# Performance work log

Measured on AMD Instinct MI355X. Metric: run time of the kernel, lower is better.

Reference implementation:

```python
import jax, jax.numpy as jnp
import numpy as np

# Grid constants from voxel_size=(0.2,0.2,4), point_cloud_range=(0,-40,-3,70.4,40,1)
VX, VY, VZ = 0.2, 0.2, 4.0
PCR = (0.0, -40.0, -3.0, 70.4, 40.0, 1.0)
NX, NY, NZ = 352, 400, 1   # round((hi-lo)/v) per axis
BATCH = 2
N_POINTS = 400000
CANVAS = BATCH * NZ * NY * NX  # dense canvas of all voxels (segment ids)
EPS = 1e-3  # BN1d eps from norm_cfg


def _vidx(coors):
    # linear voxel index: b*Z*Y*X + z*Y*X + y*X + x  (coors = [b,z,y,x])
    c = coors.astype(jnp.int32)
    return ((c[:, 0] * NZ + c[:, 1]) * NY + c[:, 2]) * NX + c[:, 3]


def _seg_mean(x, idx):
    # scatter-mean over voxels (DynamicScatter, average_points=True)
    s = jax.ops.segment_sum(x, idx, num_segments=CANVAS)
    c = jax.ops.segment_sum(jnp.ones((x.shape[0], 1), x.dtype), idx, num_segments=CANVAS)
    return s / jnp.maximum(c, 1.0)


def _seg_max(x, idx):
    # scatter-max over voxels (DynamicScatter, average_points=False); empty voxels -> 0
    m = jax.ops.segment_max(x, idx, num_segments=CANVAS)
    c = jax.ops.segment_sum(jnp.ones((x.shape[0],), x.dtype), idx, num_segments=CANVAS)
    return jnp.where((c > 0)[:, None], m, jnp.zeros_like(m))


def _bn_relu(x, g, b):
    # BN1d in training mode (batch stats, biased var), affine, then ReLU
    mu = x.mean(axis=0)
    var = x.var(axis=0)
    return jax.nn.relu((x - mu) * jax.lax.rsqrt(var + EPS) * g + b)


def setup_inputs() -> dict:
    key = jax.random.key(0)
    ks = jax.random.split(key, 6)
    features = jax.random.normal(ks[0], (N_POINTS, 4), jnp.float32)
    # coors [b, z, y, x]; batch column sorted so coors[-1,0]+1 == batch_size
    half = N_POINTS // 2
    b = jnp.concatenate([jnp.zeros(half, jnp.int32), jnp.ones(N_POINTS - half, jnp.int32)])
    z = jnp.zeros(N_POINTS, jnp.int32)  # NZ == 1
    y = jax.random.randint(ks[1], (N_POINTS,), 0, NY, jnp.int32)
    x = jax.random.randint(ks[2], (N_POINTS,), 0, NX, jnp.int32)
    coors = jnp.stack([b, z, y, x], axis=1)
    # VFE params: layer0 Linear(10->64, no bias), layer1 Linear(128->128, no bias)
    W0 = jax.random.normal(ks[3], (10, 64), jnp.float32) * 0.1
    g0 = jnp.ones((64,), jnp.float32)
    b0 = jnp.zeros((64,), jnp.float32)
    W1 = jax.random.normal(ks[4], (128, 128), jnp.float32) * 0.1
    g1 = jnp.ones((128,), jnp.float32)
    b1 = jnp.zeros((128,), jnp.float32)
    return {"features": features, "coors": coors, "W0": W0, "g0": g0, "b0": b0,
            "W1": W1, "g1": g1, "b1": b1}


def reference(features, coors, W0, g0, b0, W1, g1, b1):
    idx = _vidx(coors)
    # cluster center: scatter-mean of point features, gather back to points
    vmean = _seg_mean(features, idx)
    pts_mean = vmean[idx]
    f_cluster = features[:, :3] - pts_mean[:, :3]
    # voxel center offset
    cf = coors.astype(features.dtype)
    f_center = jnp.stack([
        features[:, 0] - (cf[:, 3] * VX + (VX / 2 + PCR[0])),
        features[:, 1] - (cf[:, 2] * VY + (VY / 2 + PCR[1])),
        features[:, 2] - (cf[:, 1] * VZ + (VZ / 2 + PCR[2])),
    ], axis=1)
    feat = jnp.concatenate([features, f_cluster, f_center], axis=1)  # (N, 10)
    # VFE layer 0 + voxel max pool + gather-broadcast + concat
    pf0 = _bn_relu(feat @ W0, g0, b0)           # (N, 64)
    v0 = _seg_max(pf0, idx)                     # (CANVAS, 64)
    feat1 = jnp.concatenate([pf0, v0[idx]], axis=1)  # (N, 128)
    # VFE layer 1 + final voxel max pool
    pf1 = _bn_relu(feat1 @ W1, g1, b1)          # (N, 128)
    voxel_feats = _seg_max(pf1, idx)            # (CANVAS, 128), dense canvas
    return voxel_feats
```

## Files before the change

kernel.cpp:

```cpp
#include <hip/hip_runtime.h>

#define NPTS 400000
#define NXv 352
#define NYv 400
#define CANVAS 281600
#define G2B 512
#define SCANB 275

typedef unsigned int uint;
typedef unsigned short ushort;
typedef __attribute__((ext_vector_type(8))) short short8;
typedef __attribute__((ext_vector_type(4))) float floatx4;

__device__ inline uint packbf(float a, float b) {
    uint ua = __float_as_uint(a);
    ua = (ua + 0x7fffu + ((ua >> 16) & 1u)) >> 16;
    uint ub = __float_as_uint(b);
    ub = (ub + 0x7fffu + ((ub >> 16) & 1u)) & 0xffff0000u;
    return ua | ub;
}
__device__ inline ushort bf16bits(float a) {
    uint u = __float_as_uint(a);
    return (ushort)((u + 0x7fffu + ((u >> 16) & 1u)) >> 16);
}
__device__ inline float lo16(uint u) { return __uint_as_float(u << 16); }
__device__ inline float hi16(uint u) { return __uint_as_float(u & 0xffff0000u); }
__device__ inline float bfval(ushort u) { return __uint_as_float(((uint)u) << 16); }

__global__ void k_bucket(const int4* __restrict__ coors, const float* __restrict__ W1,
                         int* __restrict__ idxbuf, int* __restrict__ pidx,
                         uint* __restrict__ ucnt, ushort* __restrict__ w1t) {
    int b = blockIdx.x;
    if (b < 1563) {
        int i = b * 256 + threadIdx.x;
        if (i >= NPTS) return;
        int4 c = coors[i];
        int idx = ((c.x + c.y) * NYv + c.z) * NXv + c.w;
        idxbuf[i] = idx;
        pidx[i] = (int)atomicAdd(&ucnt[idx], 1u);
    } else {
        int i = (b - 1563) * 256 + threadIdx.x;
        int n = i & 127, k = i >> 7;
        w1t[n * 128 + k] = bf16bits(W1[k * 128 + n]);
    }
}

__global__ __launch_bounds__(1024) void k_scanA(const uint* __restrict__ ucnt,
                                                uint* __restrict__ voff,
                                                uint* __restrict__ bsum) {
    __shared__ uint sh[1024];
    int t = threadIdx.x;
    int v = blockIdx.x * 1024 + t;
    uint val = ucnt[v];
    sh[t] = val;
    for (int off = 1; off < 1024; off <<= 1) {
        __syncthreads();
        uint x = (t >= off) ? sh[t - off] : 0u;
        __syncthreads();
        sh[t] += x;
    }
    uint incl = sh[t];
    voff[v] = incl - val;
    if (t == 1023) bsum[blockIdx.x] = incl;
}

__global__ __launch_bounds__(1024) void k_scanC(const uint* __restrict__ bsum,
                                                uint* __restrict__ voff) {
    __shared__ uint sh[1024];
    __shared__ uint bs[1024];
    int t = threadIdx.x;
    uint val = (t < SCANB) ? bsum[t] : 0u;
    sh[t] = val; bs[t] = val;
    for (int off = 1; off < 1024; off <<= 1) {
        __syncthreads();
        uint x = (t >= off) ? sh[t - off] : 0u;
        __syncthreads();
        sh[t] += x;
    }
    __syncthreads();
    uint off_ = sh[blockIdx.x] - bs[blockIdx.x];
    int v = blockIdx.x * 1024 + t;
    voff[v] += off_;
    if (blockIdx.x == SCANB - 1 && t == 1023) voff[CANVAS] = NPTS;
}

__global__ void k_perm(const int* __restrict__ idxbuf, const int* __restrict__ pidx,
                       const uint* __restrict__ voff, const float4* __restrict__ feat,
                       int* __restrict__ vidx, float4* __restrict__ featS) {
    int i = blockIdx.x * 256 + threadIdx.x;
    if (i >= NPTS) return;
    int idx = idxbuf[i];
    uint j = voff[idx] + (uint)pidx[i];
    vidx[j] = idx;
    featS[j] = feat[i];
}

__global__ void k_vmean(const float4* __restrict__ featS, const uint* __restrict__ voff,
                        float4* __restrict__ vmean) {
    int v = blockIdx.x * 256 + threadIdx.x;
    if (v >= CANVAS) return;
    uint s_ = voff[v], e_ = voff[v + 1];
    float4 s = make_float4(0.f, 0.f, 0.f, 0.f);
    for (uint j = s_; j < e_; ++j) {
        float4 f = featS[j];
        s.x += f.x; s.y += f.y; s.z += f.z; s.w += f.w;
    }
    float inv = 1.0f / (float)max((int)(e_ - s_), 1);
    vmean[v] = make_float4(s.x * inv, s.y * inv, s.z * inv, s.w * inv);
}

__global__ __launch_bounds__(256) void k_gemm1(
        const float4* __restrict__ featS, const int* __restrict__ vidx,
        const float4* __restrict__ vmean, const float* __restrict__ W0,
        uint* __restrict__ x0u, float* __restrict__ stats) {
    __shared__ float w0s[640];
    __shared__ __align__(8) ushort tile[256 * 68];
    __shared__ float ps[128], qs[128];
    for (int t = threadIdx.x; t < 640; t += 256) w0s[t] = W0[t];
    __syncthreads();
    int j = blockIdx.x * 256 + threadIdx.x;
    bool valid = j < NPTS;
    ushort* trow = &tile[threadIdx.x * 68];
    if (valid) {
        float4 f = featS[j];
        int idx = vidx[j];
        float4 vm = vmean[idx];
        int xq = idx % NXv;
        int yq = (idx / NXv) % NYv;
        float ft[10];
        ft[0] = f.x; ft[1] = f.y; ft[2] = f.z; ft[3] = f.w;
        ft[4] = f.x - vm.x;
        ft[5] = f.y - vm.y;
        ft[6] = f.z - vm.z;
        ft[7] = f.x - ((float)xq * 0.2f + 0.1f);
        ft[8] = f.y - ((float)yq * 0.2f - 39.9f);
        ft[9] = f.z + 1.0f;
        uint* o = x0u + (size_t)j * 32;
        #pragma unroll
        for (int g = 0; g < 8; ++g) {
            float a[8];
            #pragma unroll
            for (int q = 0; q < 8; ++q) a[q] = 0.f;
            #pragma unroll
            for (int k = 0; k < 10; ++k) {
                float fk = ft[k];
                #pragma unroll
                for (int q = 0; q < 8; ++q) a[q] = fmaf(fk, w0s[k * 64 + g * 8 + q], a[q]);
            }
            uint4 w;
            w.x = packbf(a[0], a[1]); w.y = packbf(a[2], a[3]);
            w.z = packbf(a[4], a[5]); w.w = packbf(a[6], a[7]);
            *(uint4*)(o + g * 4) = w;
            ((uint2*)trow)[g * 2 + 0] = make_uint2(w.x, w.y);
            ((uint2*)trow)[g * 2 + 1] = make_uint2(w.z, w.w);
        }
    } else {
        #pragma unroll
        for (int g = 0; g < 16; ++g) ((uint2*)trow)[g] = make_uint2(0u, 0u);
    }
    __syncthreads();
    if (threadIdx.x < 128) {
        int c = threadIdx.x & 63, half = threadIdx.x >> 6;
        float s = 0.f, q = 0.f;
        for (int r = half * 128; r < half * 128 + 128; ++r) {
            float xv = bfval(tile[r * 68 + c]);
            s += xv;
            q = fmaf(xv, xv, q);
        }
        ps[half * 64 + c] = s;
        qs[half * 64 + c] = q;
    }
    __syncthreads();
    if (threadIdx.x < 64) {
        int c = threadIdx.x;
        atomicAdd(&stats[c], ps[c] + ps[64 + c]);
        atomicAdd(&stats[64 + c], qs[c] + qs[64 + c]);
    }
}

__global__ void k_vmax0(const uint* __restrict__ x0u, const uint* __restrict__ voff,
                        const float* __restrict__ stats, const float* __restrict__ g0,
                        const float* __restrict__ b0, uint* __restrict__ v0u) {
    __shared__ float s[128];
    if (threadIdx.x < 64) {
        int c = threadIdx.x;
        float mu = stats[c] * (1.0f / NPTS);
        float var = stats[64 + c] * (1.0f / NPTS) - mu * mu;
        float sc = (1.0f / sqrtf(var + 1e-3f)) * g0[c];
        s[c] = sc;
        s[64 + c] = fmaf(-mu, sc, b0[c]);
    }
    __syncthreads();
    int t = blockIdx.x * 256 + threadIdx.x;
    int v = t >> 4;
    if (v >= CANVAS) return;
    uint s_ = voff[v], e_ = voff[v + 1];
    if (s_ == e_) return;
    int c = (t & 15) << 2;
    float4 m = make_float4(0.f, 0.f, 0.f, 0.f);
    for (uint j = s_; j < e_; ++j) {
        uint2 u = *(const uint2*)(x0u + (size_t)j * 32 + (c >> 1));
        m.x = fmaxf(m.x, fmaf(lo16(u.x), s[c + 0], s[64 + c + 0]));
        m.y = fmaxf(m.y, fmaf(hi16(u.x), s[c + 1], s[64 + c + 1]));
        m.z = fmaxf(m.z, fmaf(lo16(u.y), s[c + 2], s[64 + c + 2]));
        m.w = fmaxf(m.w, fmaf(hi16(u.y), s[c + 3], s[64 + c + 3]));
    }
    uint2 o; o.x = packbf(m.x, m.y); o.y = packbf(m.z, m.w);
    *(uint2*)(v0u + (size_t)v * 32 + (c >> 1)) = o;
}

__global__ __launch_bounds__(256) void k_gemm2p(
        const uint* __restrict__ x0u, const uint* __restrict__ v0u,
        const int* __restrict__ vidx, const uint* __restrict__ voff,
        const float* __restrict__ stats, const float* __restrict__ g0,
        const float* __restrict__ b0, const ushort* __restrict__ w1t,
        ushort* __restrict__ vmaxc, float* __restrict__ sums) {
    __shared__ __align__(16) ushort Bs[128 * 136];
    __shared__ __align__(16) ushort As[64 * 136];
    __shared__ __align__(16) ushort Cs[64 * 136];
    __shared__ float s[128];
    __shared__ int svid[2][64];

    for (int i = threadIdx.x; i < 2048; i += 256) {
        int r = i >> 4, ch = i & 15;
        *(uint4*)&Bs[r * 136 + ch * 8] = *(const uint4*)&w1t[r * 128 + ch * 8];
    }
    if (threadIdx.x < 64) {
        int c = threadIdx.x;
        float mu = stats[c] * (1.0f / NPTS);
        float var = stats[64 + c] * (1.0f / NPTS) - mu * mu;
        float sc = (1.0f / sqrtf(var + 1e-3f)) * g0[c];
        s[c] = sc;
        s[64 + c] = fmaf(-mu, sc, b0[c]);
    }

    int p0 = (int)((long long)blockIdx.x * NPTS / G2B);
    int p1 = (int)((long long)(blockIdx.x + 1) * NPTS / G2B);
    int ps, pe;
    { int v = vidx[p0]; ps = (voff[v] == (uint)p0) ? p0 : (int)voff[v + 1]; }
    if (p1 >= NPTS) pe = NPTS;
    else { int v = vidx[p1]; pe = (voff[v] == (uint)p1) ? p1 : (int)voff[v + 1]; }

    int lane = threadIdx.x & 63, wid = threadIdx.x >> 6;
    int m = lane & 15, q = lane >> 4;
    float run = -3.0e38f, csum = 0.f, csq = 0.f;
    int vcur = -1;
    __syncthreads();

    int sp = 0;
    for (int r0 = ps; r0 < pe; r0 += 64, sp ^= 1) {
        int nrows = min(64, pe - r0);
        for (int i = threadIdx.x; i < 512; i += 256) {
            int r = i >> 3, ch = i & 7, cb = ch * 8;
            uint4 o4 = make_uint4(0u, 0u, 0u, 0u);
            if (r < nrows) {
                uint4 u = *(const uint4*)(x0u + (size_t)(r0 + r) * 32 + ch * 4);
                uint w[4] = {u.x, u.y, u.z, u.w}, o[4];
                #pragma unroll
                for (int q2 = 0; q2 < 4; ++q2) {
                    float a = fmaxf(fmaf(lo16(w[q2]), s[cb + 2 * q2], s[64 + cb + 2 * q2]), 0.f);
                    float b = fmaxf(fmaf(hi16(w[q2]), s[cb + 2 * q2 + 1], s[64 + cb + 2 * q2 + 1]), 0.f);
                    o[q2] = packbf(a, b);
                }
                o4 = make_uint4(o[0], o[1], o[2], o[3]);
            }
            *(uint4*)&As[r * 136 + ch * 8] = o4;
        }
        for (int i = threadIdx.x; i < 512; i += 256) {
            int r = i >> 3, ch = i & 7;
            uint4 u = make_uint4(0u, 0u, 0u, 0u);
            if (r < nrows) u = *(const uint4*)(v0u + (size_t)vidx[r0 + r] * 32 + ch * 4);
            *(uint4*)&As[r * 136 + 64 + ch * 8] = u;
        }
        if (threadIdx.x < 64)
            svid[sp][threadIdx.x] = (threadIdx.x < nrows) ? vidx[r0 + threadIdx.x] : -1;
        __syncthreads();

        const ushort* ar = &As[(wid * 16 + m) * 136 + q * 8];
        short8 a0 = *(const short8*)&ar[0];
        short8 a1 = *(const short8*)&ar[32];
        short8 a2 = *(const short8*)&ar[64];
        short8 a3 = *(const short8*)&ar[96];
        #pragma unroll
        for (int ct = 0; ct < 8; ++ct) {
            const ushort* br = &Bs[(ct * 16 + m) * 136 + q * 8];
            short8 b0v = *(const short8*)&br[0];
            short8 b1v = *(const short8*)&br[32];
            short8 b2v = *(const short8*)&br[64];
            short8 b3v = *(const short8*)&br[96];
            floatx4 acc = {0.f, 0.f, 0.f, 0.f};
            acc = __builtin_amdgcn_mfma_f32_16x16x32_bf16(a0, b0v, acc, 0, 0, 0);
            acc = __builtin_amdgcn_mfma_f32_16x16x32_bf16(a1, b1v, acc, 0, 0, 0);
            acc = __builtin_amdgcn_mfma_f32_16x16x32_bf16(a2, b2v, acc, 0, 0, 0);
            acc = __builtin_amdgcn_mfma_f32_16x16x32_bf16(a3, b3v, acc, 0, 0, 0);
            #pragma unroll
            for (int rg = 0; rg < 4; ++rg)
                Cs[(wid * 16 + q * 4 + rg) * 136 + ct * 16 + m] = bf16bits(acc[rg]);
        }
        __syncthreads();

        if (threadIdx.x < 128) {
            int c = threadIdx.x;
            #pragma unroll 4
            for (int r = 0; r < 64; ++r) {
                int v = svid[sp][r];
                float x = bfval(Cs[r * 136 + c]);
                if (v != vcur) {
                    if (vcur >= 0) vmaxc[(size_t)vcur * 128 + c] = bf16bits(run);
                    vcur = v;
                    run = -3.0e38f;
                }
                if (v >= 0) {
                    run = fmaxf(run, x);
                    csum += x;
                    csq = fmaf(x, x, csq);
                }
            }
        }
    }
    if (threadIdx.x < 128) {
        if (vcur >= 0) vmaxc[(size_t)vcur * 128 + threadIdx.x] = bf16bits(run);
        atomicAdd(&sums[threadIdx.x], csum);
        atomicAdd(&sums[128 + threadIdx.x], csq);
    }
}

__global__ __launch_bounds__(256) void k_bnout(const ushort* __restrict__ vmaxc,
        const uint* __restrict__ voff, const float* __restrict__ stats,
        const float* __restrict__ g1, const float* __restrict__ b1,
        float4* __restrict__ out) {
    __shared__ float s[256];
    if (threadIdx.x < 128) {
        int c = threadIdx.x;
        float mu = stats[128 + c] * (1.0f / NPTS);
        float var = stats[256 + c] * (1.0f / NPTS) - mu * mu;
        float sc = (1.0f / sqrtf(var + 1e-3f)) * g1[c];
        s[c] = sc;
        s[128 + c] = fmaf(-mu, sc, b1[c]);
    }
    __syncthreads();
    int t = blockIdx.x * 256 + threadIdx.x;
    int v = t >> 5;
    if (v >= CANVAS) return;
    int c = (t & 31) << 2;
    float4 m = make_float4(0.f, 0.f, 0.f, 0.f);
    if (voff[v + 1] != voff[v]) {
        uint2 u = *(const uint2*)(vmaxc + (size_t)v * 128 + c);
        m.x = fmaxf(fmaf(lo16(u.x), s[c + 0], s[128 + c + 0]), 0.f);
        m.y = fmaxf(fmaf(hi16(u.x), s[c + 1], s[128 + c + 1]), 0.f);
        m.z = fmaxf(fmaf(lo16(u.y), s[c + 2], s[128 + c + 2]), 0.f);
        m.w = fmaxf(fmaf(hi16(u.y), s[c + 3], s[128 + c + 3]), 0.f);
    }
    out[(size_t)v * 32 + (c >> 2)] = m;
}

extern "C" void kernel_launch(void* const* d_in, const int* in_sizes, int n_in,
                              void* d_out, int out_size, void* d_ws, size_t ws_size,
                              hipStream_t stream) {
    const float4* feat  = (const float4*)d_in[0];
    const int4*   coors = (const int4*)d_in[1];
    const float*  W0    = (const float*)d_in[2];
    const float*  g0    = (const float*)d_in[3];
    const float*  b0    = (const float*)d_in[4];
    const float*  W1    = (const float*)d_in[5];
    const float*  g1    = (const float*)d_in[6];
    const float*  b1    = (const float*)d_in[7];

    char* ws = (char*)d_ws;
    int*    idxbuf = (int*)(ws + 0);
    int*    pidx   = (int*)(ws + 1600000);
    uint*   ucnt   = (uint*)(ws + 3200000);
    float*  stats  = (float*)(ws + 4326400);
    uint*   voff   = (uint*)(ws + 4329472);
    uint*   bsum   = (uint*)(ws + 5455888);
    int*    vidx   = (int*)(ws + 5459984);
    float*  featS  = (float*)(ws + 7059984);
    float*  vmean  = (float*)(ws + 13459984);
    ushort* w1t    = (ushort*)(ws + 17965584);
    uint*   x0u    = (uint*)(ws + 17998352);
    uint*   v0u    = (uint*)(ws + 69198352);
    ushort* vmaxc  = (ushort*)(ws + 105243152);

    hipMemsetAsync(ws + 3200000, 0, 1129472, stream);

    const int BLK = 256;
    int gpts = (NPTS + BLK - 1) / BLK;
    int gvox = (CANVAS + BLK - 1) / BLK;

    k_bucket<<<gpts + 64, BLK, 0, stream>>>(coors, W1, idxbuf, pidx, ucnt, w1t);
    k_scanA<<<SCANB, 1024, 0, stream>>>(ucnt, voff, bsum);
    k_scanC<<<SCANB, 1024, 0, stream>>>(bsum, voff);
    k_perm<<<gpts, BLK, 0, stream>>>(idxbuf, pidx, voff, feat, vidx, (float4*)featS);
    k_vmean<<<gvox, BLK, 0, stream>>>((const float4*)featS, voff, (float4*)vmean);
    k_gemm1<<<gpts, BLK, 0, stream>>>((const float4*)featS, vidx, (const float4*)vmean,
                                      W0, x0u, stats);
    k_vmax0<<<CANVAS * 16 / BLK, BLK, 0, stream>>>(x0u, voff, stats, g0, b0, v0u);
    k_gemm2p<<<G2B, BLK, 0, stream>>>(x0u, v0u, vidx, voff, stats, g0, b0, w1t,
                                      vmaxc, stats + 128);
    k_bnout<<<CANVAS * 32 / BLK, BLK, 0, stream>>>(vmaxc, voff, stats, g1, b1,
                                                   (float4*)d_out);
}
```

Before: 478.9 us.

## Hold W1 in registers and overlap next-tile staging with voxel max reduction

The second VFE GEMM kernel now loads each wave's W1 fragments directly into registers once, instead of copying W1 into LDS and re-reading it for every tile. Work within the block is specialized: threads 0-127 stage the next 64-row tile (BN0+ReLU of pf0 plus the gathered voxel max) while threads 128-255 run the per-voxel max and the BN-statistics reduction on the current tile. The reduction loop is also made branch-light by resetting the running max inline. The cost is about 128 extra VGPRs per thread, which may lower occupancy, and an extra barrier per tile.

Result: faster. 449.4 us (-6.2%).

```diff
diff --git a/kernel.cpp b/kernel.cpp
--- a/kernel.cpp
+++ b/kernel.cpp
@@ -215,16 +215,14 @@
         const float* __restrict__ stats, const float* __restrict__ g0,
         const float* __restrict__ b0, const ushort* __restrict__ w1t,
         ushort* __restrict__ vmaxc, float* __restrict__ sums) {
-    __shared__ __align__(16) ushort Bs[128 * 136];
     __shared__ __align__(16) ushort As[64 * 136];
     __shared__ __align__(16) ushort Cs[64 * 136];
     __shared__ float s[128];
     __shared__ int svid[2][64];
 
-    for (int i = threadIdx.x; i < 2048; i += 256) {
-        int r = i >> 4, ch = i & 15;
-        *(uint4*)&Bs[r * 136 + ch * 8] = *(const uint4*)&w1t[r * 128 + ch * 8];
-    }
+    int lane = threadIdx.x & 63, wid = threadIdx.x >> 6;
+    int m = lane & 15, q = lane >> 4;
+
     if (threadIdx.x < 64) {
         int c = threadIdx.x;
         float mu = stats[c] * (1.0f / NPTS);
@@ -234,6 +232,15 @@
         s[64 + c] = fmaf(-mu, sc, b0[c]);
     }
 
+    short8 breg[8][4];
+    #pragma unroll
+    for (int ct = 0; ct < 8; ++ct) {
+        const ushort* br = &w1t[(ct * 16 + m) * 128 + q * 8];
+        #pragma unroll
+        for (int ks = 0; ks < 4; ++ks)
+            breg[ct][ks] = *(const short8*)&br[ks * 32];
+    }
+
     int p0 = (int)((long long)blockIdx.x * NPTS / G2B);
     int p1 = (int)((long long)(blockIdx.x + 1) * NPTS / G2B);
     int ps, pe;
@@ -241,20 +248,16 @@
     if (p1 >= NPTS) pe = NPTS;
     else { int v = vidx[p1]; pe = (voff[v] == (uint)p1) ? p1 : (int)voff[v + 1]; }
 
-    int lane = threadIdx.x & 63, wid = threadIdx.x >> 6;
-    int m = lane & 15, q = lane >> 4;
     float run = -3.0e38f, csum = 0.f, csq = 0.f;
     int vcur = -1;
-    __syncthreads();
-
-    int sp = 0;
-    for (int r0 = ps; r0 < pe; r0 += 64, sp ^= 1) {
-        int nrows = min(64, pe - r0);
-        for (int i = threadIdx.x; i < 512; i += 256) {
+
+    auto stage = [&](int r0s, int p) {
+        int nrows = min(64, pe - r0s);
+        for (int i = threadIdx.x; i < 512; i += 128) {
             int r = i >> 3, ch = i & 7, cb = ch * 8;
             uint4 o4 = make_uint4(0u, 0u, 0u, 0u);
             if (r < nrows) {
-                uint4 u = *(const uint4*)(x0u + (size_t)(r0 + r) * 32 + ch * 4);
+                uint4 u = *(const uint4*)(x0u + (size_t)(r0s + r) * 32 + ch * 4);
                 uint w[4] = {u.x, u.y, u.z, u.w}, o[4];
                 #pragma unroll
                 for (int q2 = 0; q2 < 4; ++q2) {
@@ -266,16 +269,22 @@
             }
             *(uint4*)&As[r * 136 + ch * 8] = o4;
         }
-        for (int i = threadIdx.x; i < 512; i += 256) {
+        for (int i = threadIdx.x; i < 512; i += 128) {
             int r = i >> 3, ch = i & 7;
             uint4 u = make_uint4(0u, 0u, 0u, 0u);
-            if (r < nrows) u = *(const uint4*)(v0u + (size_t)vidx[r0 + r] * 32 + ch * 4);
+            if (r < nrows) u = *(const uint4*)(v0u + (size_t)vidx[r0s + r] * 32 + ch * 4);
             *(uint4*)&As[r * 136 + 64 + ch * 8] = u;
         }
         if (threadIdx.x < 64)
-            svid[sp][threadIdx.x] = (threadIdx.x < nrows) ? vidx[r0 + threadIdx.x] : -1;
-        __syncthreads();
-
+            svid[p][threadIdx.x] = (threadIdx.x < nrows) ? vidx[r0s + threadIdx.x] : -1;
+    };
+
+    __syncthreads();
+    if (threadIdx.x < 128 && ps < pe) stage(ps, 0);
+    __syncthreads();
+
+    int sp = 0;
+    for (int r0 = ps; r0 < pe; r0 += 64, sp ^= 1) {
         const ushort* ar = &As[(wid * 16 + m) * 136 + q * 8];
         short8 a0 = *(const short8*)&ar[0];
         short8 a1 = *(const short8*)&ar[32];
@@ -283,16 +292,11 @@
         short8 a3 = *(const short8*)&ar[96];
         #pragma unroll
         for (int ct = 0; ct < 8; ++ct) {
-            const ushort* br = &Bs[(ct * 16 + m) * 136 + q * 8];
-            short8 b0v = *(const short8*)&br[0];
-            short8 b1v = *(const short8*)&br[32];
-            short8 b2v = *(const short8*)&br[64];
-            short8 b3v = *(const short8*)&br[96];
             floatx4 acc = {0.f, 0.f, 0.f, 0.f};
-            acc = __builtin_amdgcn_mfma_f32_16x16x32_bf16(a0, b0v, acc, 0, 0, 0);
-            acc = __builtin_amdgcn_mfma_f32_16x16x32_bf16(a1, b1v, acc, 0, 0, 0);
-            acc = __builtin_amdgcn_mfma_f32_16x16x32_bf16(a2, b2v, acc, 0, 0, 0);
-            acc = __builtin_amdgcn_mfma_f32_16x16x32_bf16(a3, b3v, acc, 0, 0, 0);
+            acc = __builtin_amdgcn_mfma_f32_16x16x32_bf16(a0, breg[ct][0], acc, 0, 0, 0);
+            acc = __builtin_amdgcn_mfma_f32_16x16x32_bf16(a1, breg[ct][1], acc, 0, 0, 0);
+            acc = __builtin_amdgcn_mfma_f32_16x16x32_bf16(a2, breg[ct][2], acc, 0, 0, 0);
+            acc = __builtin_amdgcn_mfma_f32_16x16x32_bf16(a3, breg[ct][3], acc, 0, 0, 0);
             #pragma unroll
             for (int rg = 0; rg < 4; ++rg)
                 Cs[(wid * 16 + q * 4 + rg) * 136 + ct * 16 + m] = bf16bits(acc[rg]);
@@ -300,28 +304,30 @@
         __syncthreads();
 
         if (threadIdx.x < 128) {
-            int c = threadIdx.x;
-            #pragma unroll 4
+            if (r0 + 64 < pe) stage(r0 + 64, sp ^ 1);
+        } else {
+            int c = threadIdx.x - 128;
+            #pragma unroll 8
             for (int r = 0; r < 64; ++r) {
                 int v = svid[sp][r];
                 float x = bfval(Cs[r * 136 + c]);
-                if (v != vcur) {
-                    if (vcur >= 0) vmaxc[(size_t)vcur * 128 + c] = bf16bits(run);
-                    vcur = v;
-                    run = -3.0e38f;
-                }
-                if (v >= 0) {
-                    run = fmaxf(run, x);
-                    csum += x;
-                    csq = fmaf(x, x, csq);
-                }
+                bool brk = (v != vcur);
+                if (brk && vcur >= 0)
+                    vmaxc[(size_t)vcur * 128 + c] = bf16bits(run);
+                run = brk ? x : fmaxf(run, x);
+                vcur = v;
+                csum += x;
+                csq = fmaf(x, x, csq);
             }
         }
-    }
-    if (threadIdx.x < 128) {
-        if (vcur >= 0) vmaxc[(size_t)vcur * 128 + threadIdx.x] = bf16bits(run);
-        atomicAdd(&sums[threadIdx.x], csum);
-        atomicAdd(&sums[128 + threadIdx.x], csq);
+        __syncthreads();
+    }
+
+    if (threadIdx.x >= 128) {
+        int c = threadIdx.x - 128;
+        if (vcur >= 0) vmaxc[(size_t)vcur * 128 + c] = bf16bits(run);
+        atomicAdd(&sums[c], csum);
+        atomicAdd(&sums[128 + c], csq);
     }
 }
 
```
